# Optimization experiments

Measured on AMD Instinct MI355X. Metric: run time of the kernel, lower is better.

## Reference

```python
import jax, jax.numpy as jnp
import numpy as np

NHID = 256
NHEADS = 8
HEAD_F = NHID // NHEADS  # GAT per-head out_features
ALPHA = 0.1              # GAT LeakyReLU slope
NEG = -9e15


def _leaky(x, slope):
    return jnp.where(x >= 0, x, slope * x)


def _cnorm(x, axis):
    # matches Norm.compute_norm: (x - mean) / (std_unbiased + 1e-6)
    m = jnp.mean(x, axis=axis, keepdims=True)
    s = jnp.std(x, axis=axis, keepdims=True, ddof=1)
    return (x - m) / (s + 1e-6)


def _norm(x):
    # Norm('bn') forward: per-sample normalize over features (dim=1 of x[i]) then nodes (dim=0)
    return _cnorm(_cnorm(x, axis=2), axis=1)


def setup_inputs() -> dict:
    key = jax.random.key(0)
    ks = jax.random.split(key, 12)
    B, N, E, H, D = 4, 1024, NHID, NHEADS, HEAD_F

    def xavier(k, shape, gain=1.414):
        fan_in, fan_out = shape[-2], shape[-1]
        a = gain * np.sqrt(6.0 / (fan_in + fan_out))
        return jax.random.uniform(k, shape, jnp.float32, -a, a)

    return {
        "x": jax.random.normal(ks[0], (B, N, E), jnp.float32),
        "src": jax.random.normal(ks[1], (N, B, E), jnp.float32),
        "adj": jax.random.randint(ks[2], (B, N, N), 0, 2, jnp.int32),
        "Wg": xavier(ks[3], (H, E, D)),                 # per-head GAT W
        "a1": xavier(ks[4], (H, D, 1))[..., 0],         # a[:D]
        "a2": xavier(ks[5], (H, D, 1))[..., 0],         # a[D:]
        "lin_w": xavier(ks[6], (E, E), gain=1.0),
        "lin_b": jnp.zeros((E,), jnp.float32),
        "in_proj_w": xavier(ks[7], (3 * E, E), gain=1.0),
        "in_proj_b": jnp.zeros((3 * E,), jnp.float32),
        "out_proj_w": xavier(ks[8], (E, E), gain=1.0),
        "out_proj_b": jnp.zeros((E,), jnp.float32),
    }


def reference(x, src, adj, Wg, a1, a2, lin_w, lin_b, in_proj_w, in_proj_b, out_proj_w, out_proj_b):
    B, N, E = x.shape
    H, D = NHEADS, HEAD_F

    # --- multi-head dense GAT (all heads vectorized) ---
    Wh = jnp.einsum("bnf,hfd->hbnd", x, Wg)                      # [H,B,N,D]
    s1 = jnp.einsum("hbnd,hd->hbn", Wh, a1)                      # a1 . Wh_i
    s2 = jnp.einsum("hbnd,hd->hbn", Wh, a2)                      # a2 . Wh_j
    e = _leaky(s1[..., :, None] + s2[..., None, :], ALPHA)       # [H,B,N,N]
    e = jnp.where(adj[None] > 0, e, NEG)
    attn = jax.nn.softmax(e, axis=-1)                            # [H,B,N,N]
    hp = _leaky(jnp.einsum("hbnm,hbmd->hbnd", attn, Wh), 0.01)   # F.leaky_relu default

    x = x + jnp.transpose(hp, (1, 2, 0, 3)).reshape(B, N, H * D)
    e_out = jnp.mean(attn, axis=0)                               # [B,N,N]

    # --- norm1 -> linear -> norm2 ---
    x = _norm(x) @ lin_w.T + lin_b
    x = _norm(x)

    # --- nn.MultiheadAttention(query=x, key=x, value=src) ---
    srcb = jnp.transpose(src, (1, 0, 2))                         # [B,N,E]
    Wq, Wk, Wv = in_proj_w[:E], in_proj_w[E:2 * E], in_proj_w[2 * E:]
    bq, bk, bv = in_proj_b[:E], in_proj_b[E:2 * E], in_proj_b[2 * E:]
    Dh = E // H
    q = (x @ Wq.T + bq).reshape(B, N, H, Dh)
    k = (x @ Wk.T + bk).reshape(B, N, H, Dh)
    v = (srcb @ Wv.T + bv).reshape(B, N, H, Dh)
    scores = jnp.einsum("bqhd,bkhd->bhqk", q, k) / jnp.sqrt(jnp.float32(Dh))
    p = jax.nn.softmax(scores, axis=-1)
    o = jnp.einsum("bhqk,bkhd->bqhd", p, v).reshape(B, N, E)
    x = o @ out_proj_w.T + out_proj_b                            # [B,N,E]

    return (x, e_out)
```

## Files before the change

kernel.cpp:

```cpp
#include <hip/hip_runtime.h>
#include <hip/hip_bf16.h>

#define BIAS_OFF 196608
#define S1_OFF   198400
#define S2_OFF   231168
#define CS_OFF   263936
#define ST1_OFF  296704
#define ST2_OFF  298752
#define A_OFF    300800
#define MX_OFF   825088
#define RS_OFF   857856
#define PK_OFF   890624
#define B_OFF    1349376
#define C_OFF    2397952
#define FLAG_F   3446528

#define NEGC (-9.0e15f)

typedef __attribute__((ext_vector_type(8))) short bf16x8s;
typedef __attribute__((ext_vector_type(4))) float f32x4;

static __device__ __forceinline__ float bf2f(unsigned short u) {
  union { unsigned int i; float f; } v; v.i = ((unsigned int)u) << 16; return v.f;
}
static __device__ __forceinline__ unsigned short f2bf(float f) {
  union { float f; unsigned int u; } v; v.f = f;
  unsigned int r = (v.u + 0x7FFFu + ((v.u >> 16) & 1u)) >> 16;
  return (unsigned short)r;
}
static __device__ __forceinline__ float ldin(const void* p, long i, int bf) {
  return bf ? bf2f(((const unsigned short*)p)[i]) : ((const float*)p)[i];
}
static __device__ __forceinline__ unsigned short rdbf(const void* p, long i, int bf) {
  if (bf) return ((const unsigned short*)p)[i];
  return f2bf(((const float*)p)[i]);
}
static __device__ __forceinline__ void stout(void* p, long i, float v, int bf) {
  if (bf) ((unsigned short*)p)[i] = f2bf(v);
  else    ((float*)p)[i] = v;
}

__global__ __launch_bounds__(64) void detect_kernel(const unsigned short* x, int* flag) {
  int lane = threadIdx.x;
  unsigned short u = x[2 * lane];
  int e = (u >> 7) & 0xFF;
  bool good = (e >= 100 && e <= 140);
  unsigned long long m = __ballot(good);
  if (lane == 0) *flag = (__popcll(m) >= 48) ? 1 : 0;
}

__global__ __launch_bounds__(256) void packadj_kernel(const int* adj,
                                                      unsigned long long* pk) {
  int t = threadIdx.x, w = t >> 6, lane = t & 63;
  long row = blockIdx.x;
  #pragma unroll
  for (int j = 0; j < 4; ++j) {
    int m = t + 256*j;
    bool bit = adj[row*1024 + m] > 0;
    unsigned long long mask = __ballot(bit);
    if (lane == 0) pk[row*16 + w + 4*j] = mask;
  }
}

__global__ __launch_bounds__(256) void prep_kernel(
    const void* wg, const void* lin_w, const void* inp_w, const void* out_w,
    const void* lin_b, const void* inp_b, const void* out_b,
    const void* a1, const void* a2, float* ws, const int* flagp) {
  const int bf = *flagp;
  unsigned short* wbf = (unsigned short*)ws;
  int t = threadIdx.x;
  int f = blockIdx.x;
  int m = blockIdx.y;
  if (m == 0) {
    int h = t >> 5, d = t & 31;
    int dst = ((f >> 2)*256 + t)*4 + (f & 3);
    wbf[dst] = rdbf(wg, h*8192 + f*32 + d, bf);
  } else if (m <= 5) {
    int dst = m*65536 + t*256 + f;
    if (m == 1)      wbf[dst] = rdbf(lin_w, t*256 + f, bf);
    else if (m == 2) wbf[dst] = rdbf(inp_w, t*256 + f, bf);
    else if (m == 3) wbf[dst] = rdbf(inp_w, (256 + t)*256 + f, bf);
    else if (m == 4) wbf[dst] = rdbf(inp_w, (512 + t)*256 + f, bf);
    else             wbf[dst] = rdbf(out_w, t*256 + f, bf);
  } else if (f == 0) {
    ws[BIAS_OFF + t]        = ldin(lin_b, t, bf);
    ws[BIAS_OFF + 256 + t]  = ldin(inp_b, t, bf);
    ws[BIAS_OFF + 512 + t]  = ldin(inp_b, 256 + t, bf);
    ws[BIAS_OFF + 768 + t]  = ldin(inp_b, 512 + t, bf);
    ws[BIAS_OFF + 1024 + t] = ldin(out_b, t, bf);
    ws[BIAS_OFF + 1280 + t] = ldin(a1, t, bf);
    ws[BIAS_OFF + 1536 + t] = ldin(a2, t, bf);
  }
}

__global__ __launch_bounds__(256) void whs_kernel(const void* x, float* ws,
                                                  const int* flagp) {
  const int bf = *flagp;
  int t = threadIdx.x;
  int r0 = blockIdx.x * 8;
  __shared__ __align__(16) float U[8][256];
  #pragma unroll
  for (int r = 0; r < 8; ++r)
    U[r][t] = ldin(x, (long)(r0 + r)*256 + t, bf);
  __syncthreads();
  const ushort4* w4 = (const ushort4*)ws;
  float acc[8] = {0,0,0,0,0,0,0,0};
  for (int e4 = 0; e4 < 64; ++e4) {
    ushort4 u = w4[e4*256 + t];
    float w0 = bf2f(u.x), w1 = bf2f(u.y), w2 = bf2f(u.z), w3 = bf2f(u.w);
    #pragma unroll
    for (int r = 0; r < 8; ++r) {
      float4 uu = *(const float4*)&U[r][e4*4];
      acc[r] += uu.x*w0 + uu.y*w1 + uu.z*w2 + uu.w*w3;
    }
  }
  int h = t >> 5, d = t & 31;
  float a1v = ws[BIAS_OFF + 1280 + t];
  float a2v = ws[BIAS_OFF + 1536 + t];
  unsigned short wvals[8];
  #pragma unroll
  for (int r = 0; r < 8; ++r) {
    int row = r0 + r;
    wvals[r] = f2bf(acc[r]);
    float p1 = acc[r]*a1v, p2 = acc[r]*a2v;
    #pragma unroll
    for (int off = 16; off > 0; off >>= 1) {
      p1 += __shfl_xor(p1, off, 32);
      p2 += __shfl_xor(p2, off, 32);
    }
    if (d == 0) {
      ws[S1_OFF + h*4096 + row] = p1;
      ws[S2_OFF + h*4096 + row] = p2;
    }
  }
  {
    unsigned short* wht = (unsigned short*)(ws + A_OFF);
    int bb = r0 >> 10, nn = r0 & 1023;
    *(bf16x8s*)(wht + ((long)((h*4 + bb)*32 + d))*1024 + nn) = *(bf16x8s*)wvals;
  }
}

#define PB_S 1032
__global__ __launch_bounds__(512) void attn1a_kernel(const void* x, float* ws,
                                                     const int* flagp) {
  const int bf = *flagp;
  int t = threadIdx.x;
  int gid = blockIdx.x;
  int h = gid & 7;
  int b = (gid >> 3) & 3;
  int n0 = (gid >> 5) * 16;
  __shared__ __align__(16) float s2s[1024];
  __shared__ __align__(16) unsigned short Pb[16][PB_S];
  __shared__ __align__(16) float opart[8][16][17];
  int w = t >> 6, lane = t & 63;
  int m = lane & 15, quad = lane >> 4;
  const unsigned long long* pk = (const unsigned long long*)(ws + PK_OFF);
  const float* s2p = ws + S2_OFF + h*4096 + b*1024;
  #pragma unroll
  for (int j = 0; j < 2; ++j) s2s[t + 512*j] = s2p[t + 512*j];
  __syncthreads();
  #pragma unroll
  for (int rr = 0; rr < 2; ++rr) {
    int r = 2*w + rr;
    int rowi = __builtin_amdgcn_readfirstlane(b*1024 + n0 + r);
    const unsigned long long* prow = pk + (long)rowi * 16;
    float s1v = ws[S1_OFF + h*4096 + rowi];
    float p[16];
    float mx = -3.4e38f;
    #pragma unroll
    for (int j = 0; j < 16; ++j) {
      int mm = lane + 64*j;
      float ev = s1v + s2s[mm];
      ev = (ev >= 0.0f) ? ev : 0.1f*ev;
      ev = ((prow[j] >> lane) & 1ull) ? ev : NEGC;
      p[j] = ev;
      mx = fmaxf(mx, ev);
    }
    #pragma unroll
    for (int off = 32; off > 0; off >>= 1) mx = fmaxf(mx, __shfl_xor(mx, off));
    float s = 0.0f;
    #pragma unroll
    for (int j = 0; j < 16; ++j) { p[j] = __expf(p[j] - mx); s += p[j]; }
    #pragma unroll
    for (int off = 32; off > 0; off >>= 1) s += __shfl_xor(s, off);
    float rs = 1.0f / s;
    #pragma unroll
    for (int j = 0; j < 16; ++j)
      Pb[r][lane + 64*j] = f2bf(p[j] * rs);
    if (lane == 0) {
      ws[MX_OFF + h*4096 + rowi] = mx;
      ws[RS_OFF + h*4096 + rowi] = rs;
    }
  }
  __syncthreads();
  {
    const unsigned short* wht = (const unsigned short*)(ws + A_OFF);
    int ntile = w & 1;
    int ktbase = (w >> 1) * 8;
    int vd = ntile*16 + m;
    const unsigned short* wrow = wht + ((long)((h*4 + b)*32 + vd))*1024;
    f32x4 acc0 = {0.0f, 0.0f, 0.0f, 0.0f};
    f32x4 acc1 = {0.0f, 0.0f, 0.0f, 0.0f};
    #pragma unroll
    for (int kt2 = 0; kt2 < 4; ++kt2) {
      int kt = ktbase + 2*kt2;
      bf16x8s ap0 = *(const bf16x8s*)&Pb[m][kt*32 + quad*8];
      bf16x8s bw0 = *(const bf16x8s*)(wrow + kt*32 + quad*8);
      acc0 = __builtin_amdgcn_mfma_f32_16x16x32_bf16(ap0, bw0, acc0, 0, 0, 0);
      bf16x8s ap1 = *(const bf16x8s*)&Pb[m][(kt+1)*32 + quad*8];
      bf16x8s bw1 = *(const bf16x8s*)(wrow + (kt+1)*32 + quad*8);
      acc1 = __builtin_amdgcn_mfma_f32_16x16x32_bf16(ap1, bw1, acc1, 0, 0, 0);
    }
    f32x4 acc = acc0 + acc1;
    #pragma unroll
    for (int i = 0; i < 4; ++i)
      opart[w][quad*4 + i][m] = acc[i];
  }
  __syncthreads();
  {
    int r = t >> 5, dd = t & 31;
    int nt = dd >> 4, c = dd & 15;
    float sum = opart[nt][r][c] + opart[nt + 2][r][c]
              + opart[nt + 4][r][c] + opart[nt + 6][r][c];
    float hv = (sum >= 0.0f) ? sum : 0.01f*sum;
    long idx = (long)(b*1024 + n0 + r)*256 + h*32 + dd;
    ws[C_OFF + idx] = ldin(x, idx, bf) + hv;
  }
}

__global__ __launch_bounds__(256) void eout_kernel(float* ws, void* dout,
                                                   const int* flagp) {
  const int bf = *flagp;
  int t = threadIdx.x;
  int gid = blockIdx.x;
  int b = gid & 3;
  int n = gid >> 2;
  int row = b*1024 + n;
  int w = t >> 6, lane = t & 63;
  __shared__ float part[8];
  const unsigned long long* pk = (const unsigned long long*)(ws + PK_OFF);
  const unsigned long long* prow = pk + (long)row * 16;
  float v = ws[C_OFF + (long)row*256 + t];
  float s = v;
  #pragma unroll
  for (int off = 32; off > 0; off >>= 1) s += __shfl_xor(s, off);
  if (lane == 0) part[w] = s;
  __syncthreads();
  float mean = (part[0] + part[1] + part[2] + part[3]) * (1.0f/256.0f);
  float d = v - mean;
  float ss = d*d;
  #pragma unroll
  for (int off = 32; off > 0; off >>= 1) ss += __shfl_xor(ss, off);
  if (lane == 0) part[4 + w] = ss;
  __syncthreads();
  float inv = 1.0f / (sqrtf((part[4]+part[5]+part[6]+part[7]) * (1.0f/255.0f)) + 1e-6f);
  ws[B_OFF + (long)row*256 + t] = d * inv;
  float s1v[8], mxv[8], rsv[8];
  #pragma unroll
  for (int h = 0; h < 8; ++h) {
    s1v[h] = ws[S1_OFF + h*4096 + row];
    mxv[h] = ws[MX_OFF + h*4096 + row];
    rsv[h] = ws[RS_OFF + h*4096 + row];
  }
  const float* s2b = ws + S2_OFF + b*1024;
  #pragma unroll
  for (int j = 0; j < 4; ++j) {
    int m = t + 256*j;
    bool a = (prow[w + 4*j] >> lane) & 1ull;
    float acc = 0.0f;
    #pragma unroll
    for (int h = 0; h < 8; ++h) {
      float ev = s1v[h] + s2b[h*4096 + m];
      ev = (ev >= 0.0f) ? ev : 0.1f*ev;
      ev = a ? ev : NEGC;
      acc += rsv[h] * __expf(ev - mxv[h]);
    }
    stout(dout, 1048576L + (long)row*1024 + m, 0.125f*acc, bf);
  }
}

__global__ __launch_bounds__(256) void colstatsA_kernel(const float* in, float* cs) {
  int t = threadIdx.x;
  int j = blockIdx.x & 63;
  int b = blockIdx.x >> 6;
  float s = 0, ss = 0;
  for (int n = j*16; n < j*16 + 16; ++n) {
    float v = in[(b*1024 + n)*256 + t];
    s += v; ss += v*v;
  }
  cs[(b*64 + j)*256 + t] = s;
  cs[65536 + (b*64 + j)*256 + t] = ss;
}

__global__ __launch_bounds__(256) void colstatsB_kernel(const float* cs, float* st) {
  int t = threadIdx.x;
  int b = blockIdx.x;
  float s = 0, ss = 0;
  for (int j = 0; j < 64; ++j) {
    s  += cs[(b*64 + j)*256 + t];
    ss += cs[65536 + (b*64 + j)*256 + t];
  }
  float mean = s * (1.0f/1024.0f);
  float var = fmaxf((ss - s*mean) * (1.0f/1023.0f), 0.0f);
  st[b*256 + t] = mean;
  st[1024 + b*256 + t] = 1.0f / (sqrtf(var) + 1e-6f);
}

template<int IN_MODE, int RN, int OUTM, int CS>
__global__ __launch_bounds__(512) void gemm2_kernel(const void* inp,
    const unsigned short* wmat, const unsigned short* wmat2,
    const float* bias, const float* bias2, const float* st,
    void* outp, const int* flagp) {
  const int bf = *flagp;
  int t = threadIdx.x;
  int gid = blockIdx.x;
  int rowg = (CS == 2) ? (gid >> 1) : gid;
  int colbase = (CS == 2) ? ((gid & 1) * 128) : 0;
  int r0 = rowg * 16;
  __shared__ __align__(16) unsigned short Usm[2*16*264];
  unsigned short (*Uh)[264] = (unsigned short (*)[264])Usm;
  unsigned short (*Ul)[264] = (unsigned short (*)[264])(Usm + 16*264);
  {
    int srow = t >> 5;
    int e0 = (t & 31) * 8;
    long grow = r0 + srow;
    float v[8];
    if (IN_MODE == 1) {
      int b = (int)(grow >> 10);
      const float* ip = (const float*)inp + grow*256 + e0;
      const float* mp = st + b*256 + e0;
      const float* vp = st + 1024 + b*256 + e0;
      #pragma unroll
      for (int j = 0; j < 8; ++j) v[j] = (ip[j] - mp[j]) * vp[j];
    } else if (IN_MODE == 2) {
      int b = (int)(grow >> 10), n = (int)(grow & 1023);
      #pragma unroll
      for (int j = 0; j < 8; ++j)
        v[j] = ldin(inp, (long)(n*4 + b)*256 + e0 + j, bf);
    } else {
      int b = (int)(grow >> 10), n = (int)(grow & 1023);
      const float* ip = (const float*)inp
          + ((long)(b*8 + (e0 >> 5))*1024 + n)*32 + (e0 & 31);
      #pragma unroll
      for (int j = 0; j < 8; ++j) v[j] = ip[j];
    }
    unsigned short hv[8], lv[8];
    #pragma unroll
    for (int j = 0; j < 8; ++j) {
      hv[j] = f2bf(v[j]);
      lv[j] = f2bf(v[j] - bf2f(hv[j]));
    }
    *(bf16x8s*)&Uh[srow][e0] = *(bf16x8s*)hv;
    *(bf16x8s*)&Ul[srow][e0] = *(bf16x8s*)lv;
  }
  __syncthreads();
  int w = t >> 6, lane = t & 63, m = lane & 15, quad = lane >> 4;
  const int NT = (CS == 1) ? 2 : 1;
  f32x4 accs[2];
  f32x4 acck;
  #pragma unroll
  for (int nt = 0; nt < NT; ++nt) {
    int o = colbase + w*16 + nt*128 + m;
    const unsigned short* wp = wmat + o*256 + quad*8;
    f32x4 ah_acc = {0,0,0,0}, al_acc = {0,0,0,0};
    f32x4 kh_acc = {0,0,0,0}, kl_acc = {0,0,0,0};
    const unsigned short* wp2 = (OUTM == 5) ? (wmat2 + o*256 + quad*8) : wp;
    #pragma unroll
    for (int kt = 0; kt < 8; ++kt) {
      bf16x8s ah = *(const bf16x8s*)&Uh[m][kt*32 + quad*8];
      bf16x8s al = *(const bf16x8s*)&Ul[m][kt*32 + quad*8];
      bf16x8s bw = *(const bf16x8s*)(wp + kt*32);
      ah_acc = __builtin_amdgcn_mfma_f32_16x16x32_bf16(ah, bw, ah_acc, 0, 0, 0);
      al_acc = __builtin_amdgcn_mfma_f32_16x16x32_bf16(al, bw, al_acc, 0, 0, 0);
      if (OUTM == 5) {
        bf16x8s bw2 = *(const bf16x8s*)(wp2 + kt*32);
        kh_acc = __builtin_amdgcn_mfma_f32_16x16x32_bf16(ah, bw2, kh_acc, 0, 0, 0);
        kl_acc = __builtin_amdgcn_mfma_f32_16x16x32_bf16(al, bw2, kl_acc, 0, 0, 0);
      }
    }
    accs[nt] = ah_acc + al_acc;
    if (OUTM == 5) acck = kh_acc + kl_acc;
    if (RN == 0) {
      float bv = bias[o];
      if constexpr (OUTM == 0) {
        #pragma unroll
        for (int i = 0; i < 4; ++i) {
          long row = r0 + quad*4 + i;
          ((float*)outp)[row*256 + o] = accs[nt][i] + bv;
        }
      } else if constexpr (OUTM == 1) {
        #pragma unroll
        for (int i = 0; i < 4; ++i) {
          long row = r0 + quad*4 + i;
          stout(outp, row*256 + o, accs[nt][i] + bv, bf);
        }
      } else if constexpr (OUTM == 4) {
        int h = o >> 5, d = o & 31;
        #pragma unroll
        for (int i = 0; i < 4; ++i) {
          long row = r0 + quad*4 + i;
          int b = (int)(row >> 10), n = (int)(row & 1023);
          ((unsigned short*)outp)[((long)((b*8 + h)*32 + d))*1024 + n]
              = f2bf(accs[nt][i] + bv);
        }
      } else if constexpr (OUTM == 5) {
        float* wsf = (float*)outp;
        float* qhm = wsf + A_OFF;
        unsigned short* khm = (unsigned short*)(wsf + B_OFF);
        float bq = bias[o], bk = bias2[o];
        int h = o >> 5, d = o & 31;
        #pragma unroll
        for (int i = 0; i < 4; ++i) {
          long row = r0 + quad*4 + i;
          int b = (int)(row >> 10), n = (int)(row & 1023);
          long idx = ((long)((b*8 + h)*1024 + n))*32 + d;
          qhm[idx] = accs[nt][i] + bq;
          khm[idx] = f2bf(acck[i] + bk);
        }
      }
    }
  }
  if constexpr (RN == 1) {
    __syncthreads();
    float (*O)[264] = (float (*)[264])Usm;
    #pragma unroll
    for (int nt = 0; nt < NT; ++nt) {
      int oc = colbase + w*16 + nt*128 + m;
      float bv = bias[oc];
      #pragma unroll
      for (int i = 0; i < 4; ++i)
        O[quad*4 + i][oc] = accs[nt][i] + bv;
    }
    __syncthreads();
    #pragma unroll
    for (int rr = 0; rr < 2; ++rr) {
      int r = 2*w + rr;
      float vals[4]; float s = 0.0f;
      #pragma unroll
      for (int j = 0; j < 4; ++j) { vals[j] = O[r][lane + 64*j]; s += vals[j]; }
      #pragma unroll
      for (int off = 32; off > 0; off >>= 1) s += __shfl_xor(s, off);
      float mean = s * (1.0f/256.0f);
      float ss = 0.0f;
      #pragma unroll
      for (int j = 0; j < 4; ++j) { float d = vals[j] - mean; ss += d*d; }
      #pragma unroll
      for (int off = 32; off > 0; off >>= 1) ss += __shfl_xor(ss, off);
      float inv = 1.0f / (sqrtf(ss * (1.0f/255.0f)) + 1e-6f);
      #pragma unroll
      for (int j = 0; j < 4; ++j)
        ((float*)outp)[(long)(r0 + r)*256 + lane + 64*j] = (vals[j] - mean) * inv;
    }
  }
}

#define SPS 1036
__global__ __launch_bounds__(512) void attn2_kernel(float* ws) {
  int t = threadIdx.x;
  int gid = blockIdx.x;
  int h = gid & 7;
  int b = (gid >> 3) & 3;
  int n0 = (gid >> 5) << 4;
  __shared__ __align__(16) float Sp[16*SPS];
  __shared__ __align__(16) float opart[8][16][17];
  float* qq = ws + A_OFF;
  const unsigned short* kk = (const unsigned short*)(ws + B_OFF);
  const unsigned short* vt = (const unsigned short*)(ws + C_OFF);
  int base_bh = (b*8 + h)*1024;
  int w = t >> 6, lane = t & 63;
  int m = lane & 15, quad = lane >> 4;
  const float scl = 0.17677669529663687f;
  {
    const float* qp = qq + (base_bh + n0 + m)*32 + quad*8;
    bf16x8s aq;
    #pragma unroll
    for (int j = 0; j < 8; ++j) ((unsigned short*)&aq)[j] = f2bf(qp[j]);
    f32x4 zero = {0.0f, 0.0f, 0.0f, 0.0f};
    #pragma unroll
    for (int kt = 0; kt < 8; ++kt) {
      int kbase = w*128 + kt*16;
      bf16x8s bk = *(const bf16x8s*)(kk + (base_bh + kbase + m)*32 + quad*8);
      f32x4 d = __builtin_amdgcn_mfma_f32_16x16x32_bf16(aq, bk, zero, 0, 0, 0);
      int key = kbase + m;
      #pragma unroll
      for (int i = 0; i < 4; ++i)
        Sp[(quad*4 + i)*SPS + key] = d[i] * scl;
    }
  }
  __syncthreads();
  #pragma unroll
  for (int rr = 0; rr < 2; ++rr) {
    int r = 2*w + rr;
    float* Sr = Sp + r*SPS;
    float p[16];
    #pragma unroll
    for (int j = 0; j < 16; ++j) p[j] = Sr[lane + 64*j];
    float mx = -3.4e38f;
    #pragma unroll
    for (int j = 0; j < 16; ++j) mx = fmaxf(mx, p[j]);
    #pragma unroll
    for (int off = 32; off > 0; off >>= 1) mx = fmaxf(mx, __shfl_xor(mx, off));
    float s = 0.0f;
    #pragma unroll
    for (int j = 0; j < 16; ++j) { p[j] = __expf(p[j] - mx); s += p[j]; }
    #pragma unroll
    for (int off = 32; off > 0; off >>= 1) s += __shfl_xor(s, off);
    float rs = 1.0f / s;
    unsigned short* Pr = (unsigned short*)Sr;
    #pragma unroll
    for (int j = 0; j < 16; ++j)
      Pr[lane + 64*j] = f2bf(p[j] * rs);
  }
  __syncthreads();
  {
    int ntile = w & 1;
    int ktbase = (w >> 1) * 8;
    int vd = ntile*16 + m;
    const unsigned short* vrow = vt + base_bh*32 + vd*1024;
    const unsigned short* P0 = (const unsigned short*)Sp + m*(SPS*2);
    f32x4 acc0 = {0.0f, 0.0f, 0.0f, 0.0f};
    f32x4 acc1 = {0.0f, 0.0f, 0.0f, 0.0f};
    #pragma unroll
    for (int kt2 = 0; kt2 < 4; ++kt2) {
      int kt = ktbase + 2*kt2;
      bf16x8s ap0 = *(const bf16x8s*)(P0 + kt*32 + quad*8);
      bf16x8s bv0 = *(const bf16x8s*)(vrow + kt*32 + quad*8);
      acc0 = __builtin_amdgcn_mfma_f32_16x16x32_bf16(ap0, bv0, acc0, 0, 0, 0);
      bf16x8s ap1 = *(const bf16x8s*)(P0 + (kt+1)*32 + quad*8);
      bf16x8s bv1 = *(const bf16x8s*)(vrow + (kt+1)*32 + quad*8);
      acc1 = __builtin_amdgcn_mfma_f32_16x16x32_bf16(ap1, bv1, acc1, 0, 0, 0);
    }
    f32x4 acc = acc0 + acc1;
    #pragma unroll
    for (int i = 0; i < 4; ++i)
      opart[w][quad*4 + i][m] = acc[i];
  }
  __syncthreads();
  {
    int r = t >> 5, d = t & 31;
    int nt = d >> 4, c = d & 15;
    float sum = opart[nt][r][c] + opart[nt + 2][r][c]
              + opart[nt + 4][r][c] + opart[nt + 6][r][c];
    qq[(base_bh + n0 + r)*32 + d] = sum;
  }
}

extern "C" void kernel_launch(void* const* d_in, const int* in_sizes, int n_in,
                              void* d_out, int out_size, void* d_ws, size_t ws_size,
                              hipStream_t stream) {
  const void* x   = d_in[0];
  const void* src = d_in[1];
  const int* adj  = (const int*)d_in[2];
  const void* wg  = d_in[3];
  const void* a1  = d_in[4];
  const void* a2  = d_in[5];
  const void* lw  = d_in[6];
  const void* lb  = d_in[7];
  const void* ipw = d_in[8];
  const void* ipb = d_in[9];
  const void* opw = d_in[10];
  const void* opb = d_in[11];
  float* ws = (float*)d_ws;
  const unsigned short* wbf = (const unsigned short*)d_ws;
  int* flagp = (int*)(ws + FLAG_F);

  detect_kernel<<<1, 64, 0, stream>>>((const unsigned short*)x, flagp);
  prep_kernel<<<dim3(256, 7), 256, 0, stream>>>(wg, lw, ipw, opw, lb, ipb, opb,
                                                a1, a2, ws, flagp);
  packadj_kernel<<<4096, 256, 0, stream>>>(adj,
      (unsigned long long*)(ws + PK_OFF));
  whs_kernel<<<512, 256, 0, stream>>>(x, ws, flagp);
  attn1a_kernel<<<2048, 512, 0, stream>>>(x, ws, flagp);
  eout_kernel<<<4096, 256, 0, stream>>>(ws, d_out, flagp);
  colstatsA_kernel<<<256, 256, 0, stream>>>(ws + B_OFF, ws + MX_OFF);
  colstatsB_kernel<<<4, 256, 0, stream>>>(ws + MX_OFF, ws + ST1_OFF);
  gemm2_kernel<1,1,0,1><<<256, 512, 0, stream>>>(ws + B_OFF, wbf + 1*65536,
      nullptr, ws + BIAS_OFF, nullptr, ws + ST1_OFF, ws + C_OFF, flagp);
  colstatsA_kernel<<<256, 256, 0, stream>>>(ws + C_OFF, ws + MX_OFF);
  colstatsB_kernel<<<4, 256, 0, stream>>>(ws + MX_OFF, ws + ST2_OFF);
  gemm2_kernel<1,0,5,2><<<512, 512, 0, stream>>>(ws + C_OFF, wbf + 2*65536,
      wbf + 3*65536, ws + BIAS_OFF + 256, ws + BIAS_OFF + 512, ws + ST2_OFF,
      ws, flagp);
  gemm2_kernel<2,0,4,2><<<512, 512, 0, stream>>>(src, wbf + 4*65536,
      nullptr, ws + BIAS_OFF + 768, nullptr, nullptr, ws + C_OFF, flagp);
  attn2_kernel<<<2048, 512, 0, stream>>>(ws);
  gemm2_kernel<3,0,1,2><<<512, 512, 0, stream>>>(ws + A_OFF, wbf + 5*65536,
      nullptr, ws + BIAS_OFF + 1024, nullptr, nullptr, d_out, flagp);
}
```

Baseline: 255.2 us.

## Replace scalar Wh projection with MFMA GEMM, precompute folded attention vectors, double attn1a rows

The scalar whs_kernel is dropped. Wh is now produced by the existing MFMA gemm2 kernel in a new raw-input mode, and s1/s2 come from a small kernel that dots x with Wg·a1 and Wg·a2 vectors folded together in prep. attn1a now handles 32 rows per block with a shared LDS arena, so each Wh load feeds two MFMA row groups and half as many blocks are launched. The post-linear norm gemm also writes per-block column sums and sums of squares, which removes the second colstatsA launch. The cost is an extra kernel launch, s1/s2 computed from folded weights with different rounding, and higher LDS use per attn1a block.

Measured after the change: 245.6 us. 1.04x faster.

```diff
diff --git a/kernel.cpp b/kernel.cpp
--- a/kernel.cpp
+++ b/kernel.cpp
@@ -73,8 +73,7 @@
   int m = blockIdx.y;
   if (m == 0) {
     int h = t >> 5, d = t & 31;
-    int dst = ((f >> 2)*256 + t)*4 + (f & 3);
-    wbf[dst] = rdbf(wg, h*8192 + f*32 + d, bf);
+    wbf[t*256 + f] = rdbf(wg, h*8192 + f*32 + d, bf);
   } else if (m <= 5) {
     int dst = m*65536 + t*256 + f;
     if (m == 1)      wbf[dst] = rdbf(lin_w, t*256 + f, bf);
@@ -82,62 +81,51 @@
     else if (m == 3) wbf[dst] = rdbf(inp_w, (256 + t)*256 + f, bf);
     else if (m == 4) wbf[dst] = rdbf(inp_w, (512 + t)*256 + f, bf);
     else             wbf[dst] = rdbf(out_w, t*256 + f, bf);
-  } else if (f == 0) {
-    ws[BIAS_OFF + t]        = ldin(lin_b, t, bf);
-    ws[BIAS_OFF + 256 + t]  = ldin(inp_b, t, bf);
-    ws[BIAS_OFF + 512 + t]  = ldin(inp_b, 256 + t, bf);
-    ws[BIAS_OFF + 768 + t]  = ldin(inp_b, 512 + t, bf);
-    ws[BIAS_OFF + 1024 + t] = ldin(out_b, t, bf);
-    ws[BIAS_OFF + 1280 + t] = ldin(a1, t, bf);
-    ws[BIAS_OFF + 1536 + t] = ldin(a2, t, bf);
-  }
-}
-
-__global__ __launch_bounds__(256) void whs_kernel(const void* x, float* ws,
-                                                  const int* flagp) {
-  const int bf = *flagp;
-  int t = threadIdx.x;
-  int r0 = blockIdx.x * 8;
-  __shared__ __align__(16) float U[8][256];
-  #pragma unroll
-  for (int r = 0; r < 8; ++r)
-    U[r][t] = ldin(x, (long)(r0 + r)*256 + t, bf);
-  __syncthreads();
-  const ushort4* w4 = (const ushort4*)ws;
-  float acc[8] = {0,0,0,0,0,0,0,0};
-  for (int e4 = 0; e4 < 64; ++e4) {
-    ushort4 u = w4[e4*256 + t];
-    float w0 = bf2f(u.x), w1 = bf2f(u.y), w2 = bf2f(u.z), w3 = bf2f(u.w);
-    #pragma unroll
-    for (int r = 0; r < 8; ++r) {
-      float4 uu = *(const float4*)&U[r][e4*4];
-      acc[r] += uu.x*w0 + uu.y*w1 + uu.z*w2 + uu.w*w3;
-    }
-  }
-  int h = t >> 5, d = t & 31;
-  float a1v = ws[BIAS_OFF + 1280 + t];
-  float a2v = ws[BIAS_OFF + 1536 + t];
-  unsigned short wvals[8];
-  #pragma unroll
-  for (int r = 0; r < 8; ++r) {
-    int row = r0 + r;
-    wvals[r] = f2bf(acc[r]);
-    float p1 = acc[r]*a1v, p2 = acc[r]*a2v;
+  } else {
+    int h = t >> 5, d = t & 31;
+    float wv = ldin(wg, h*8192 + f*32 + d, bf);
+    float p1 = wv * ldin(a1, t, bf);
+    float p2 = wv * ldin(a2, t, bf);
     #pragma unroll
     for (int off = 16; off > 0; off >>= 1) {
       p1 += __shfl_xor(p1, off, 32);
       p2 += __shfl_xor(p2, off, 32);
     }
     if (d == 0) {
-      ws[S1_OFF + h*4096 + row] = p1;
-      ws[S2_OFF + h*4096 + row] = p2;
-    }
-  }
-  {
-    unsigned short* wht = (unsigned short*)(ws + A_OFF);
-    int bb = r0 >> 10, nn = r0 & 1023;
-    *(bf16x8s*)(wht + ((long)((h*4 + bb)*32 + d))*1024 + nn) = *(bf16x8s*)wvals;
-  }
+      ws[CS_OFF + h*256 + f]        = p1;
+      ws[CS_OFF + 2048 + h*256 + f] = p2;
+    }
+    if (f == 0) {
+      ws[BIAS_OFF + t]        = ldin(lin_b, t, bf);
+      ws[BIAS_OFF + 256 + t]  = ldin(inp_b, t, bf);
+      ws[BIAS_OFF + 512 + t]  = ldin(inp_b, 256 + t, bf);
+      ws[BIAS_OFF + 768 + t]  = ldin(inp_b, 512 + t, bf);
+      ws[BIAS_OFF + 1024 + t] = ldin(out_b, t, bf);
+      ws[CS_OFF + 4096 + t]   = 0.0f;
+    }
+  }
+}
+
+__global__ __launch_bounds__(256) void s1s2_kernel(const void* x, float* ws,
+                                                   const int* flagp) {
+  const int bf = *flagp;
+  int t = threadIdx.x;
+  int r0 = blockIdx.x * 16;
+  __shared__ float X[16][260];
+  __shared__ float CA[16][260];
+  #pragma unroll
+  for (int r = 0; r < 16; ++r)
+    X[r][t] = ldin(x, (long)(r0 + r)*256 + t, bf);
+  #pragma unroll
+  for (int i = 0; i < 16; ++i)
+    CA[i][t] = ws[CS_OFF + ((i < 8) ? i*256 : 2048 + (i - 8)*256) + t];
+  __syncthreads();
+  int r = t >> 4, c = t & 15;
+  float acc = 0.0f;
+  for (int e = 0; e < 256; ++e) acc += X[r][e] * CA[c][e];
+  int row = r0 + r;
+  if (c < 8) ws[S1_OFF + c*4096 + row] = acc;
+  else       ws[S2_OFF + (c - 8)*4096 + row] = acc;
 }
 
 #define PB_S 1032
@@ -148,10 +136,11 @@
   int gid = blockIdx.x;
   int h = gid & 7;
   int b = (gid >> 3) & 3;
-  int n0 = (gid >> 5) * 16;
-  __shared__ __align__(16) float s2s[1024];
-  __shared__ __align__(16) unsigned short Pb[16][PB_S];
-  __shared__ __align__(16) float opart[8][16][17];
+  int n0 = (gid >> 5) * 32;
+  __shared__ __align__(16) unsigned char arena[4096 + 32*PB_S*2];
+  float* s2s = (float*)arena;
+  unsigned short (*Pb)[PB_S] = (unsigned short (*)[PB_S])(arena + 4096);
+  float (*opart)[32][17] = (float (*)[32][17])arena;
   int w = t >> 6, lane = t & 63;
   int m = lane & 15, quad = lane >> 4;
   const unsigned long long* pk = (const unsigned long long*)(ws + PK_OFF);
@@ -160,8 +149,8 @@
   for (int j = 0; j < 2; ++j) s2s[t + 512*j] = s2p[t + 512*j];
   __syncthreads();
   #pragma unroll
-  for (int rr = 0; rr < 2; ++rr) {
-    int r = 2*w + rr;
+  for (int rr = 0; rr < 4; ++rr) {
+    int r = 4*w + rr;
     int rowi = __builtin_amdgcn_readfirstlane(b*1024 + n0 + r);
     const unsigned long long* prow = pk + (long)rowi * 16;
     float s1v = ws[S1_OFF + h*4096 + rowi];
@@ -193,32 +182,43 @@
     }
   }
   __syncthreads();
+  f32x4 g0, g1;
   {
     const unsigned short* wht = (const unsigned short*)(ws + A_OFF);
     int ntile = w & 1;
     int ktbase = (w >> 1) * 8;
     int vd = ntile*16 + m;
-    const unsigned short* wrow = wht + ((long)((h*4 + b)*32 + vd))*1024;
-    f32x4 acc0 = {0.0f, 0.0f, 0.0f, 0.0f};
-    f32x4 acc1 = {0.0f, 0.0f, 0.0f, 0.0f};
+    const unsigned short* wrow = wht + ((long)((b*8 + h)*32 + vd))*1024;
+    f32x4 a0g0 = {0,0,0,0}, a1g0 = {0,0,0,0};
+    f32x4 a0g1 = {0,0,0,0}, a1g1 = {0,0,0,0};
     #pragma unroll
     for (int kt2 = 0; kt2 < 4; ++kt2) {
       int kt = ktbase + 2*kt2;
-      bf16x8s ap0 = *(const bf16x8s*)&Pb[m][kt*32 + quad*8];
       bf16x8s bw0 = *(const bf16x8s*)(wrow + kt*32 + quad*8);
-      acc0 = __builtin_amdgcn_mfma_f32_16x16x32_bf16(ap0, bw0, acc0, 0, 0, 0);
-      bf16x8s ap1 = *(const bf16x8s*)&Pb[m][(kt+1)*32 + quad*8];
       bf16x8s bw1 = *(const bf16x8s*)(wrow + (kt+1)*32 + quad*8);
-      acc1 = __builtin_amdgcn_mfma_f32_16x16x32_bf16(ap1, bw1, acc1, 0, 0, 0);
-    }
-    f32x4 acc = acc0 + acc1;
-    #pragma unroll
-    for (int i = 0; i < 4; ++i)
-      opart[w][quad*4 + i][m] = acc[i];
-  }
-  __syncthreads();
-  {
-    int r = t >> 5, dd = t & 31;
+      bf16x8s p00 = *(const bf16x8s*)&Pb[m][kt*32 + quad*8];
+      bf16x8s p01 = *(const bf16x8s*)&Pb[16 + m][kt*32 + quad*8];
+      a0g0 = __builtin_amdgcn_mfma_f32_16x16x32_bf16(p00, bw0, a0g0, 0, 0, 0);
+      a0g1 = __builtin_amdgcn_mfma_f32_16x16x32_bf16(p01, bw0, a0g1, 0, 0, 0);
+      bf16x8s p10 = *(const bf16x8s*)&Pb[m][(kt+1)*32 + quad*8];
+      bf16x8s p11 = *(const bf16x8s*)&Pb[16 + m][(kt+1)*32 + quad*8];
+      a1g0 = __builtin_amdgcn_mfma_f32_16x16x32_bf16(p10, bw1, a1g0, 0, 0, 0);
+      a1g1 = __builtin_amdgcn_mfma_f32_16x16x32_bf16(p11, bw1, a1g1, 0, 0, 0);
+    }
+    g0 = a0g0 + a1g0;
+    g1 = a0g1 + a1g1;
+  }
+  __syncthreads();
+  #pragma unroll
+  for (int i = 0; i < 4; ++i) {
+    opart[w][quad*4 + i][m]      = g0[i];
+    opart[w][16 + quad*4 + i][m] = g1[i];
+  }
+  __syncthreads();
+  #pragma unroll
+  for (int half = 0; half < 2; ++half) {
+    int r = (t >> 5) + half*16;
+    int dd = t & 31;
     int nt = dd >> 4, c = dd & 15;
     float sum = opart[nt][r][c] + opart[nt + 2][r][c]
               + opart[nt + 4][r][c] + opart[nt + 6][r][c];
@@ -310,7 +310,7 @@
 __global__ __launch_bounds__(512) void gemm2_kernel(const void* inp,
     const unsigned short* wmat, const unsigned short* wmat2,
     const float* bias, const float* bias2, const float* st,
-    void* outp, const int* flagp) {
+    void* outp, float* csout, const int* flagp) {
   const int bf = *flagp;
   int t = threadIdx.x;
   int gid = blockIdx.x;
@@ -325,7 +325,10 @@
     int e0 = (t & 31) * 8;
     long grow = r0 + srow;
     float v[8];
-    if (IN_MODE == 1) {
+    if (IN_MODE == 0) {
+      #pragma unroll
+      for (int j = 0; j < 8; ++j) v[j] = ldin(inp, grow*256 + e0 + j, bf);
+    } else if (IN_MODE == 1) {
       int b = (int)(grow >> 10);
       const float* ip = (const float*)inp + grow*256 + e0;
       const float* mp = st + b*256 + e0;
@@ -448,8 +451,19 @@
       for (int off = 32; off > 0; off >>= 1) ss += __shfl_xor(ss, off);
       float inv = 1.0f / (sqrtf(ss * (1.0f/255.0f)) + 1e-6f);
       #pragma unroll
-      for (int j = 0; j < 4; ++j)
-        ((float*)outp)[(long)(r0 + r)*256 + lane + 64*j] = (vals[j] - mean) * inv;
+      for (int j = 0; j < 4; ++j) {
+        float nv = (vals[j] - mean) * inv;
+        ((float*)outp)[(long)(r0 + r)*256 + lane + 64*j] = nv;
+        O[r][lane + 64*j] = nv;
+      }
+    }
+    __syncthreads();
+    if (csout != nullptr && t < 256) {
+      float s = 0, ss = 0;
+      #pragma unroll
+      for (int r = 0; r < 16; ++r) { float v = O[r][t]; s += v; ss += v*v; }
+      csout[gid*256 + t] = s;
+      csout[65536 + gid*256 + t] = ss;
     }
   }
 }
@@ -569,21 +583,26 @@
                                                 a1, a2, ws, flagp);
   packadj_kernel<<<4096, 256, 0, stream>>>(adj,
       (unsigned long long*)(ws + PK_OFF));
-  whs_kernel<<<512, 256, 0, stream>>>(x, ws, flagp);
-  attn1a_kernel<<<2048, 512, 0, stream>>>(x, ws, flagp);
+  gemm2_kernel<0,0,4,2><<<512, 512, 0, stream>>>(x, wbf + 0*65536,
+      nullptr, ws + CS_OFF + 4096, nullptr, nullptr, ws + A_OFF, nullptr,
+      flagp);
+  s1s2_kernel<<<256, 256, 0, stream>>>(x, ws, flagp);
+  attn1a_kernel<<<1024, 512, 0, stream>>>(x, ws, flagp);
   eout_kernel<<<4096, 256, 0, stream>>>(ws, d_out, flagp);
   colstatsA_kernel<<<256, 256, 0, stream>>>(ws + B_OFF, ws + MX_OFF);
   colstatsB_kernel<<<4, 256, 0, stream>>>(ws + MX_OFF, ws + ST1_OFF);
   gemm2_kernel<1,1,0,1><<<256, 512, 0, stream>>>(ws + B_OFF, wbf + 1*65536,
-      nullptr, ws + BIAS_OFF, nullptr, ws + ST1_OFF, ws + C_OFF, flagp);
-  colstatsA_kernel<<<256, 256, 0, stream>>>(ws + C_OFF, ws + MX_OFF);
+      nullptr, ws + BIAS_OFF, nullptr, ws + ST1_OFF, ws + C_OFF, ws + MX_OFF,
+      flagp);
   colstatsB_kernel<<<4, 256, 0, stream>>>(ws + MX_OFF, ws + ST2_OFF);
   gemm2_kernel<1,0,5,2><<<512, 512, 0, stream>>>(ws + C_OFF, wbf + 2*65536,
       wbf + 3*65536, ws + BIAS_OFF + 256, ws + BIAS_OFF + 512, ws + ST2_OFF,
-      ws, flagp);
+      ws, nullptr, flagp);
   gemm2_kernel<2,0,4,2><<<512, 512, 0, stream>>>(src, wbf + 4*65536,
-      nullptr, ws + BIAS_OFF + 768, nullptr, nullptr, ws + C_OFF, flagp);
+      nullptr, ws + BIAS_OFF + 768, nullptr, nullptr, ws + C_OFF, nullptr,
+      flagp);
   attn2_kernel<<<2048, 512, 0, stream>>>(ws);
   gemm2_kernel<3,0,1,2><<<512, 512, 0, stream>>>(ws + A_OFF, wbf + 5*65536,
-      nullptr, ws + BIAS_OFF + 1024, nullptr, nullptr, d_out, flagp);
-}
+      nullptr, ws + BIAS_OFF + 1024, nullptr, nullptr, d_out, nullptr,
+      flagp);
+}
```
